# Performance work log

Hardware: AMD Instinct MI355X
Metric: run time of the kernel (lower is better)

## Reference

```python
import jax, jax.numpy as jnp
import numpy as np

B, S, D, H = 4, 2048, 512, 8
HD = D // H  # head_size = 64


def setup_inputs() -> dict:
    key = jax.random.key(0)
    ks = jax.random.split(key, 11)
    sd = 1.0 / np.sqrt(D)
    return {
        "q": jax.random.normal(ks[0], (B, S, D), jnp.float32),
        "k": jax.random.normal(ks[1], (B, S, D), jnp.float32),
        "v": jax.random.normal(ks[2], (B, S, D), jnp.float32),
        "Wq": jax.random.normal(ks[3], (D, D), jnp.float32) * sd,
        "bq": jnp.zeros((D,), jnp.float32),
        "Wk": jax.random.normal(ks[4], (D, D), jnp.float32) * sd,
        "bk": jnp.zeros((D,), jnp.float32),
        "Wv": jax.random.normal(ks[5], (D, D), jnp.float32) * sd,
        "bv": jnp.zeros((D,), jnp.float32),
        "Wo": jax.random.normal(ks[6], (D, D), jnp.float32) * sd,
        "bo": jnp.zeros((D,), jnp.float32),
    }


def _split_heads(x):
    # [B,S,D] -> [B,H,S,HD]
    return x.reshape(B, S, H, HD).transpose(0, 2, 1, 3)


def reference(q, k, v, Wq, bq, Wk, bk, Wv, bv, Wo, bo):
    qp = _split_heads(q @ Wq.T + bq)
    kp = _split_heads(k @ Wk.T + bk)
    vp = _split_heads(v @ Wv.T + bv)
    scale = 1.0 / jnp.sqrt(jnp.float32(HD))
    scores = jnp.einsum("bhqd,bhkd->bhqk", qp, kp) * scale  # [B,H,S,S]
    weights = jax.nn.softmax(scores, axis=-1)
    ctx = jnp.einsum("bhqk,bhkd->bhqd", weights, vp)
    ctx = ctx.transpose(0, 2, 1, 3).reshape(B, S, D)
    return ctx @ Wo.T + bo
```

## Files before the change

kernel.cpp:

```cpp
#include <hip/hip_runtime.h>
#include <hip/hip_bf16.h>
#include <stdint.h>

#define BB   4
#define SS   2048
#define DDIM 512
#define HH   8
#define HDIM 64
#define MTOT (BB*SS)
#define QSCALE (0.125f * 1.44269504088896340736f)

typedef __bf16 bf16;
typedef __bf16 bf16x8 __attribute__((ext_vector_type(8)));
typedef float  f32x4  __attribute__((ext_vector_type(4)));

__device__ __forceinline__ f32x4 mfma32(bf16x8 a, bf16x8 b, f32x4 c) {
    return __builtin_amdgcn_mfma_f32_16x16x32_bf16(a, b, c, 0, 0, 0);
}

__device__ __forceinline__ void gload_lds16(const void* g, void* l) {
    __builtin_amdgcn_global_load_lds(
        (__attribute__((address_space(1))) unsigned int*)(uintptr_t)g,
        (__attribute__((address_space(3))) unsigned int*)l,
        16, 0, 0);
}

__device__ __forceinline__ short bf16bits(float f) {
    union { __bf16 h; short s; } u; u.h = (__bf16)f; return u.s;
}

__global__ void cvt_kernel(const float* __restrict__ q, const float* __restrict__ k,
                           const float* __restrict__ v, const float* __restrict__ w0,
                           const float* __restrict__ w1, const float* __restrict__ w2,
                           const float* __restrict__ w3,
                           bf16* __restrict__ dq, bf16* __restrict__ dk,
                           bf16* __restrict__ dv, bf16* __restrict__ dw0,
                           bf16* __restrict__ dw1, bf16* __restrict__ dw2,
                           bf16* __restrict__ dw3) {
    const float* s; bf16* d; int n4;
    switch (blockIdx.y) {
        case 0: s = q;  d = dq;  n4 = (BB*SS*DDIM)/4; break;
        case 1: s = k;  d = dk;  n4 = (BB*SS*DDIM)/4; break;
        case 2: s = v;  d = dv;  n4 = (BB*SS*DDIM)/4; break;
        case 3: s = w0; d = dw0; n4 = (DDIM*DDIM)/4; break;
        case 4: s = w1; d = dw1; n4 = (DDIM*DDIM)/4; break;
        case 5: s = w2; d = dw2; n4 = (DDIM*DDIM)/4; break;
        default: s = w3; d = dw3; n4 = (DDIM*DDIM)/4; break;
    }
    int stride = gridDim.x * blockDim.x;
    for (int i = blockIdx.x * blockDim.x + threadIdx.x; i < n4; i += stride) {
        float4 f = ((const float4*)s)[i];
        union { bf16 h[4]; uint2 u; } o;
        o.h[0] = (bf16)f.x; o.h[1] = (bf16)f.y; o.h[2] = (bf16)f.z; o.h[3] = (bf16)f.w;
        ((uint2*)d)[i] = o.u;
    }
}

#define GEMM_BODY(A_, W_, K_, MB_, NB_)                                          \
    __shared__ bf16 As[128 * 64];                                                \
    __shared__ bf16 Bs[128 * 64];                                                \
    const int tid = threadIdx.x;                                                 \
    const int w = tid >> 6, lane = tid & 63;                                     \
    const int c15 = lane & 15, quad = lane >> 4;                                 \
    const int mblk = (MB_), nblk = (NB_);                                        \
    const int wm = (w & 1) * 64, wn = (w >> 1) * 64;                             \
    f32x4 acc[4][4] = {};                                                        \
    const bf16* Ablk = (A_) + (size_t)mblk * (K_);                               \
    const bf16* Bblk = (W_) + (size_t)nblk * (K_);                               \
    int g_off[4], l_base[4];                                                     \
    _Pragma("unroll")                                                            \
    for (int ci = 0; ci < 4; ++ci) {                                             \
        const int s = (w * 4 + ci) * 64 + lane;                                  \
        const int kr = s >> 3, kc = (s & 7) ^ (kr & 7);                          \
        g_off[ci] = kr * (K_) + kc * 8;                                          \
        l_base[ci] = (w * 4 + ci) * 512;                                         \
    }                                                                            \
    for (int kt = 0; kt < (K_); kt += 64) {                                      \
        __syncthreads();                                                         \
        _Pragma("unroll")                                                        \
        for (int ci = 0; ci < 4; ++ci) {                                         \
            gload_lds16(Ablk + g_off[ci] + kt, &As[l_base[ci]]);                 \
            gload_lds16(Bblk + g_off[ci] + kt, &Bs[l_base[ci]]);                 \
        }                                                                        \
        __syncthreads();                                                         \
        _Pragma("unroll")                                                        \
        for (int hh = 0; hh < 2; ++hh) {                                         \
            bf16x8 af[4], bfr[4];                                                \
            _Pragma("unroll")                                                    \
            for (int i = 0; i < 4; ++i) {                                        \
                const int row = wm + i * 16 + c15;                               \
                af[i] = *(const bf16x8*)&As[row * 64 + (((hh * 4 + quad) ^ (row & 7)) * 8)]; \
            }                                                                    \
            _Pragma("unroll")                                                    \
            for (int j = 0; j < 4; ++j) {                                        \
                const int row = wn + j * 16 + c15;                               \
                bfr[j] = *(const bf16x8*)&Bs[row * 64 + (((hh * 4 + quad) ^ (row & 7)) * 8)]; \
            }                                                                    \
            _Pragma("unroll")                                                    \
            for (int i = 0; i < 4; ++i)                                          \
                _Pragma("unroll")                                                \
                for (int j = 0; j < 4; ++j)                                      \
                    acc[i][j] = mfma32(af[i], bfr[j], acc[i][j]);                \
        }                                                                        \
    }

__global__ __launch_bounds__(256)
void proj_gemm(const bf16* __restrict__ Aq, const bf16* __restrict__ Ak,
               const bf16* __restrict__ Av,
               const bf16* __restrict__ Wq, const bf16* __restrict__ Wk,
               const bf16* __restrict__ Wv,
               const float* __restrict__ bq, const float* __restrict__ bk,
               const float* __restrict__ bv,
               bf16* __restrict__ Qp, bf16* __restrict__ Kp, bf16* __restrict__ Vt2) {
    const int mode = blockIdx.z;
    const bf16* A;  const bf16* Wm; const float* bias;
    int mb, nb;
    if (mode == 0)      { A = Aq; Wm = Wq; bias = bq; mb = blockIdx.x * 128; nb = blockIdx.y * 128; }
    else if (mode == 1) { A = Ak; Wm = Wk; bias = bk; mb = blockIdx.x * 128; nb = blockIdx.y * 128; }
    else {
        const int id = blockIdx.y * 64 + blockIdx.x;
        A = Wv; Wm = Av; bias = bv; mb = (id & 3) * 128; nb = (id >> 2) * 128;
    }
    GEMM_BODY(A, Wm, DDIM, mb, nb)
    if (mode == 2) {
        #pragma unroll
        for (int i = 0; i < 4; ++i) {
            #pragma unroll
            for (int r = 0; r < 4; ++r) {
                const int row = mblk + wm + i * 16 + quad * 4 + r;
                const float bval = bias[row];
                #pragma unroll
                for (int j = 0; j < 4; ++j) {
                    const int col = nblk + wn + j * 16 + c15;
                    Vt2[(size_t)row * MTOT + col] = (bf16)(acc[i][j][r] + bval);
                }
            }
        }
    } else {
        #pragma unroll
        for (int j = 0; j < 4; ++j) {
            const int col = nblk + wn + j * 16 + c15;
            const int h = col >> 6, hd = col & 63;
            const float bval = bias[col];
            #pragma unroll
            for (int i = 0; i < 4; ++i) {
                #pragma unroll
                for (int r = 0; r < 4; ++r) {
                    const int row = mblk + wm + i * 16 + quad * 4 + r;
                    const int b = row >> 11, s = row & (SS - 1);
                    float v = acc[i][j][r] + bval;
                    if (mode == 0) v *= QSCALE;
                    bf16* dst = (mode == 0) ? Qp : Kp;
                    dst[(((size_t)(b * HH + h)) * SS + s) * HDIM + hd] = (bf16)v;
                }
            }
        }
    }
}

__global__ __launch_bounds__(256)
void out_gemm(const bf16* __restrict__ A, const bf16* __restrict__ Wo,
              const float* __restrict__ bo, float* __restrict__ Out) {
    GEMM_BODY(A, Wo, DDIM, blockIdx.x * 128, blockIdx.y * 128)
    #pragma unroll
    for (int j = 0; j < 4; ++j) {
        const int col = nblk + wn + j * 16 + c15;
        const float bval = bo[col];
        #pragma unroll
        for (int i = 0; i < 4; ++i) {
            #pragma unroll
            for (int r = 0; r < 4; ++r) {
                const int row = mblk + wm + i * 16 + quad * 4 + r;
                Out[(size_t)row * DDIM + col] = acc[i][j][r] + bval;
            }
        }
    }
}

__global__ __launch_bounds__(256, 2)
void attn_kernel(const bf16* __restrict__ Qp, const bf16* __restrict__ Kp,
                 const bf16* __restrict__ Vt2, bf16* __restrict__ Ctx) {
    __shared__ bf16 Klds[128 * 64];
    __shared__ bf16 Vlds[64 * 128];

    const int tid = threadIdx.x;
    const int w = tid >> 6, lane = tid & 63;
    const int c15 = lane & 15, quad = lane >> 4;
    const int bh = blockIdx.y;
    const int b = bh >> 3, h = bh & 7;
    const int qbase = blockIdx.x * 128;

    const bf16* Qh = Qp + (size_t)bh * SS * HDIM;
    const bf16* Kh = Kp + (size_t)bh * SS * HDIM;
    const bf16* Vh = Vt2 + (size_t)h * HDIM * MTOT + (size_t)b * SS;

    bf16x8 qf[2][2];
    #pragma unroll
    for (int g = 0; g < 2; ++g) {
        const int qrow = qbase + w * 32 + g * 16 + c15;
        qf[g][0] = *(const bf16x8*)&Qh[(size_t)qrow * HDIM + quad * 8];
        qf[g][1] = *(const bf16x8*)&Qh[(size_t)qrow * HDIM + 32 + quad * 8];
    }

    int koff[4], voff[4];
    #pragma unroll
    for (int ci = 0; ci < 4; ++ci) {
        const int s = (w * 4 + ci) * 64 + lane;
        const int kr = s >> 3, kc = (s & 7) ^ (kr & 7);
        koff[ci] = kr * HDIM + kc * 8;
        const int vr = s >> 4, vc = (s & 15) ^ (vr & 15);
        voff[ci] = vr * MTOT + vc * 8;
    }

    union FragS { short s[8]; bf16x8 v; };
    FragS idf, ones8;
    #pragma unroll
    for (int j = 0; j < 8; ++j) {
        idf.s[j] = (j < 4 && quad * 4 + j == c15) ? (short)0x3F80 : (short)0;
        ones8.s[j] = (short)0x3F80;
    }

    f32x4 oacc[2][4] = {};
    f32x4 lacc[2] = {};
    const int ksw = c15 & 7;

    for (int kt = 0; kt < SS; kt += 128) {
        __syncthreads();
        const bf16* Ks = Kh + (size_t)kt * HDIM;
        const bf16* Vs = Vh + kt;
        #pragma unroll
        for (int ci = 0; ci < 4; ++ci)
            gload_lds16(Ks + koff[ci], &Klds[(w * 4 + ci) * 512]);
        #pragma unroll
        for (int ci = 0; ci < 4; ++ci)
            gload_lds16(Vs + voff[ci], &Vlds[(w * 4 + ci) * 512]);
        __syncthreads();

        FragS paf[2][4];
        #pragma unroll
        for (int nt = 0; nt < 8; ++nt) {
            const int krow = nt * 16 + c15;
            bf16x8 kb0 = *(const bf16x8*)&Klds[(krow * 8 + (quad ^ ksw)) * 8];
            bf16x8 kb1 = *(const bf16x8*)&Klds[(krow * 8 + ((quad + 4) ^ ksw)) * 8];
            #pragma unroll
            for (int g = 0; g < 2; ++g) {
                f32x4 z = {};
                z = mfma32(qf[g][0], kb0, z);
                z = mfma32(qf[g][1], kb1, z);
                FragS pk;
                #pragma unroll
                for (int r = 0; r < 4; ++r)
                    pk.s[r] = bf16bits(__builtin_amdgcn_exp2f(z[r]));
                pk.s[4] = pk.s[5] = pk.s[6] = pk.s[7] = 0;
                f32x4 zero = {};
                f32x4 t = mfma32(pk.v, idf.v, zero);
                const int half = (nt & 1) * 4;
                #pragma unroll
                for (int r = 0; r < 4; ++r)
                    paf[g][nt >> 1].s[half + r] = bf16bits(t[r]);
            }
        }

        #pragma unroll
        for (int t = 0; t < 4; ++t) {
            lacc[0] = mfma32(paf[0][t].v, ones8.v, lacc[0]);
            lacc[1] = mfma32(paf[1][t].v, ones8.v, lacc[1]);
            #pragma unroll
            for (int j = 0; j < 4; ++j) {
                const int row = j * 16 + c15;
                union { uint2 u[2]; bf16x8 v; } vb;
                vb.u[0] = *(const uint2*)&Vlds[row * 128 +
                          (((4 * t + (quad >> 1)) ^ c15) * 8) + (quad & 1) * 4];
                vb.u[1] = *(const uint2*)&Vlds[row * 128 +
                          (((4 * t + 2 + (quad >> 1)) ^ c15) * 8) + (quad & 1) * 4];
                oacc[0][j] = mfma32(paf[0][t].v, vb.v, oacc[0][j]);
                oacc[1][j] = mfma32(paf[1][t].v, vb.v, oacc[1][j]);
            }
        }
    }

    bf16* Cb = Ctx + ((size_t)b * SS) * DDIM + (size_t)h * HDIM;
    #pragma unroll
    for (int g = 0; g < 2; ++g)
        #pragma unroll
        for (int r = 0; r < 4; ++r) {
            const int row = qbase + w * 32 + g * 16 + quad * 4 + r;
            const float inv = 1.0f / lacc[g][r];
            #pragma unroll
            for (int j = 0; j < 4; ++j) {
                const int hd = j * 16 + c15;
                Cb[(size_t)row * DDIM + hd] = (bf16)(oacc[g][j][r] * inv);
            }
        }
}

extern "C" void kernel_launch(void* const* d_in, const int* in_sizes, int n_in,
                              void* d_out, int out_size, void* d_ws, size_t ws_size,
                              hipStream_t stream) {
    const float* q  = (const float*)d_in[0];
    const float* k  = (const float*)d_in[1];
    const float* v  = (const float*)d_in[2];
    const float* Wq = (const float*)d_in[3];
    const float* bq = (const float*)d_in[4];
    const float* Wk = (const float*)d_in[5];
    const float* bk = (const float*)d_in[6];
    const float* Wv = (const float*)d_in[7];
    const float* bv = (const float*)d_in[8];
    const float* Wo = (const float*)d_in[9];
    const float* bo = (const float*)d_in[10];
    float* out = (float*)d_out;

    const size_t SZ_T = (size_t)BB * SS * DDIM * 2;
    const size_t SZ_W = (size_t)DDIM * DDIM * 2;
    char* ws = (char*)d_ws;
    bf16* qb  = (bf16*)(ws + 0 * SZ_T);
    bf16* kb  = (bf16*)(ws + 1 * SZ_T);
    bf16* vb  = (bf16*)(ws + 2 * SZ_T);
    bf16* Wqb = (bf16*)(ws + 3 * SZ_T + 0 * SZ_W);
    bf16* Wkb = (bf16*)(ws + 3 * SZ_T + 1 * SZ_W);
    bf16* Wvb = (bf16*)(ws + 3 * SZ_T + 2 * SZ_W);
    bf16* Wob = (bf16*)(ws + 3 * SZ_T + 3 * SZ_W);
    bf16* Qp  = (bf16*)(ws + 3 * SZ_T + 4 * SZ_W);
    bf16* Kp  = (bf16*)(ws + 4 * SZ_T + 4 * SZ_W);
    bf16* Vt2 = (bf16*)(ws + 5 * SZ_T + 4 * SZ_W);
    bf16* ctx = (bf16*)(ws + 6 * SZ_T + 4 * SZ_W);
    const size_t needed = 7 * SZ_T + 4 * SZ_W;
    if (ws_size < needed) return;

    cvt_kernel<<<dim3(512, 7), 256, 0, stream>>>(q, k, v, Wq, Wk, Wv, Wo,
                                                 qb, kb, vb, Wqb, Wkb, Wvb, Wob);
    proj_gemm<<<dim3(MTOT / 128, DDIM / 128, 3), 256, 0, stream>>>(
        qb, kb, vb, Wqb, Wkb, Wvb, bq, bk, bv, Qp, Kp, Vt2);
    attn_kernel<<<dim3(SS / 128, BB * HH), 256, 0, stream>>>(Qp, Kp, Vt2, ctx);
    out_gemm<<<dim3(MTOT / 128, DDIM / 128), 256, 0, stream>>>(ctx, Wob, bo, out);
}
```

Measured before the change: 193.9 us.

## Double-buffer LDS tiles in GEMM and attention, permute V layout for wide loads

Both the projection GEMM and the attention kernel now use two LDS buffers. The next K-tile's global-to-LDS load is issued before computing on the current one, which removes one barrier per iteration and overlaps memory latency with MFMA work. The V-projection epilogue also stores columns in a permuted order, so the attention kernel can read each V fragment with one 16-byte LDS load instead of two 8-byte loads. The cost is double the LDS per block, which may limit occupancy. Correctness also depends on the barrier waiting for the async LDS loads to finish.

```diff
diff --git a/kernel.cpp b/kernel.cpp
--- a/kernel.cpp
+++ b/kernel.cpp
@@ -57,8 +57,8 @@
 }
 
 #define GEMM_BODY(A_, W_, K_, MB_, NB_)                                          \
-    __shared__ bf16 As[128 * 64];                                                \
-    __shared__ bf16 Bs[128 * 64];                                                \
+    __shared__ bf16 As[2][128 * 64];                                             \
+    __shared__ bf16 Bs[2][128 * 64];                                             \
     const int tid = threadIdx.x;                                                 \
     const int w = tid >> 6, lane = tid & 63;                                     \
     const int c15 = lane & 15, quad = lane >> 4;                                 \
@@ -75,26 +75,33 @@
         g_off[ci] = kr * (K_) + kc * 8;                                          \
         l_base[ci] = (w * 4 + ci) * 512;                                         \
     }                                                                            \
+    _Pragma("unroll")                                                            \
+    for (int ci = 0; ci < 4; ++ci) {                                             \
+        gload_lds16(Ablk + g_off[ci], &As[0][l_base[ci]]);                       \
+        gload_lds16(Bblk + g_off[ci], &Bs[0][l_base[ci]]);                       \
+    }                                                                            \
+    int bufi = 0;                                                                \
     for (int kt = 0; kt < (K_); kt += 64) {                                      \
-        __syncthreads();                                                         \
-        _Pragma("unroll")                                                        \
-        for (int ci = 0; ci < 4; ++ci) {                                         \
-            gload_lds16(Ablk + g_off[ci] + kt, &As[l_base[ci]]);                 \
-            gload_lds16(Bblk + g_off[ci] + kt, &Bs[l_base[ci]]);                 \
+        __syncthreads();              \
+        if (kt + 64 < (K_)) {                                                    \
+            _Pragma("unroll")                                                    \
+            for (int ci = 0; ci < 4; ++ci) {                                     \
+                gload_lds16(Ablk + g_off[ci] + kt + 64, &As[bufi ^ 1][l_base[ci]]); \
+                gload_lds16(Bblk + g_off[ci] + kt + 64, &Bs[bufi ^ 1][l_base[ci]]); \
+            }                                                                    \
         }                                                                        \
-        __syncthreads();                                                         \
         _Pragma("unroll")                                                        \
         for (int hh = 0; hh < 2; ++hh) {                                         \
             bf16x8 af[4], bfr[4];                                                \
             _Pragma("unroll")                                                    \
             for (int i = 0; i < 4; ++i) {                                        \
                 const int row = wm + i * 16 + c15;                               \
-                af[i] = *(const bf16x8*)&As[row * 64 + (((hh * 4 + quad) ^ (row & 7)) * 8)]; \
+                af[i] = *(const bf16x8*)&As[bufi][row * 64 + (((hh * 4 + quad) ^ (row & 7)) * 8)]; \
             }                                                                    \
             _Pragma("unroll")                                                    \
             for (int j = 0; j < 4; ++j) {                                        \
                 const int row = wn + j * 16 + c15;                               \
-                bfr[j] = *(const bf16x8*)&Bs[row * 64 + (((hh * 4 + quad) ^ (row & 7)) * 8)]; \
+                bfr[j] = *(const bf16x8*)&Bs[bufi][row * 64 + (((hh * 4 + quad) ^ (row & 7)) * 8)]; \
             }                                                                    \
             _Pragma("unroll")                                                    \
             for (int i = 0; i < 4; ++i)                                          \
@@ -102,6 +109,7 @@
                 for (int j = 0; j < 4; ++j)                                      \
                     acc[i][j] = mfma32(af[i], bfr[j], acc[i][j]);                \
         }                                                                        \
+        bufi ^= 1;                                                               \
     }
 
 __global__ __launch_bounds__(256)
@@ -132,7 +140,8 @@
                 #pragma unroll
                 for (int j = 0; j < 4; ++j) {
                     const int col = nblk + wn + j * 16 + c15;
-                    Vt2[(size_t)row * MTOT + col] = (bf16)(acc[i][j][r] + bval);
+                    const int colp = (col & ~31) + (c15 >> 2) * 8 + (j & 1) * 4 + (c15 & 3);
+                    Vt2[(size_t)row * MTOT + colp] = (bf16)(acc[i][j][r] + bval);
                 }
             }
         }
@@ -180,8 +189,8 @@
 __global__ __launch_bounds__(256, 2)
 void attn_kernel(const bf16* __restrict__ Qp, const bf16* __restrict__ Kp,
                  const bf16* __restrict__ Vt2, bf16* __restrict__ Ctx) {
-    __shared__ bf16 Klds[128 * 64];
-    __shared__ bf16 Vlds[64 * 128];
+    __shared__ bf16 Klds[2][128 * 64];
+    __shared__ bf16 Vlds[2][64 * 128];
 
     const int tid = threadIdx.x;
     const int w = tid >> 6, lane = tid & 63;
@@ -224,24 +233,31 @@
     f32x4 lacc[2] = {};
     const int ksw = c15 & 7;
 
+    #pragma unroll
+    for (int ci = 0; ci < 4; ++ci) {
+        gload_lds16(Kh + koff[ci], &Klds[0][(w * 4 + ci) * 512]);
+        gload_lds16(Vh + voff[ci], &Vlds[0][(w * 4 + ci) * 512]);
+    }
+
+    int buf = 0;
     for (int kt = 0; kt < SS; kt += 128) {
         __syncthreads();
-        const bf16* Ks = Kh + (size_t)kt * HDIM;
-        const bf16* Vs = Vh + kt;
-        #pragma unroll
-        for (int ci = 0; ci < 4; ++ci)
-            gload_lds16(Ks + koff[ci], &Klds[(w * 4 + ci) * 512]);
-        #pragma unroll
-        for (int ci = 0; ci < 4; ++ci)
-            gload_lds16(Vs + voff[ci], &Vlds[(w * 4 + ci) * 512]);
-        __syncthreads();
+        if (kt + 128 < SS) {
+            const bf16* Ks = Kh + (size_t)(kt + 128) * HDIM;
+            const bf16* Vs = Vh + (kt + 128);
+            #pragma unroll
+            for (int ci = 0; ci < 4; ++ci) {
+                gload_lds16(Ks + koff[ci], &Klds[buf ^ 1][(w * 4 + ci) * 512]);
+                gload_lds16(Vs + voff[ci], &Vlds[buf ^ 1][(w * 4 + ci) * 512]);
+            }
+        }
 
         FragS paf[2][4];
         #pragma unroll
         for (int nt = 0; nt < 8; ++nt) {
             const int krow = nt * 16 + c15;
-            bf16x8 kb0 = *(const bf16x8*)&Klds[(krow * 8 + (quad ^ ksw)) * 8];
-            bf16x8 kb1 = *(const bf16x8*)&Klds[(krow * 8 + ((quad + 4) ^ ksw)) * 8];
+            bf16x8 kb0 = *(const bf16x8*)&Klds[buf][(krow * 8 + (quad ^ ksw)) * 8];
+            bf16x8 kb1 = *(const bf16x8*)&Klds[buf][(krow * 8 + ((quad + 4) ^ ksw)) * 8];
             #pragma unroll
             for (int g = 0; g < 2; ++g) {
                 f32x4 z = {};
@@ -268,15 +284,13 @@
             #pragma unroll
             for (int j = 0; j < 4; ++j) {
                 const int row = j * 16 + c15;
-                union { uint2 u[2]; bf16x8 v; } vb;
-                vb.u[0] = *(const uint2*)&Vlds[row * 128 +
-                          (((4 * t + (quad >> 1)) ^ c15) * 8) + (quad & 1) * 4];
-                vb.u[1] = *(const uint2*)&Vlds[row * 128 +
-                          (((4 * t + 2 + (quad >> 1)) ^ c15) * 8) + (quad & 1) * 4];
-                oacc[0][j] = mfma32(paf[0][t].v, vb.v, oacc[0][j]);
-                oacc[1][j] = mfma32(paf[1][t].v, vb.v, oacc[1][j]);
-            }
-        }
+                bf16x8 vb = *(const bf16x8*)&Vlds[buf][row * 128 +
+                            (((4 * t + quad) ^ c15) * 8)];
+                oacc[0][j] = mfma32(paf[0][t].v, vb, oacc[0][j]);
+                oacc[1][j] = mfma32(paf[1][t].v, vb, oacc[1][j]);
+            }
+        }
+        buf ^= 1;
     }
 
     bf16* Cb = Ctx + ((size_t)b * SS) * DDIM + (size_t)h * HDIM;
```

Result: no change. 191.6 us (-1.2%).
